# Kernel tuning notes

Measured on AMD Instinct MI355X. Metric: run time of the kernel, lower is better.

The kernel has to match this reference:

```python
import jax, jax.numpy as jnp
import numpy as np

VIN, VOUT, E, H = 32000, 32000, 1024, 1024
TS, TT, B = 50, 48, 64


def _lstm_scan(x, m, Wih, Whh, bih, bhh):
    """Masked (packed-sequence-equivalent) LSTM. x:(T,B,E), m:(T,B) bool valid."""
    Bn, Hn = x.shape[1], Whh.shape[1]

    def step(carry, tm):
        h, c = carry
        xt, mt = tm
        gates = xt @ Wih.T + bih + h @ Whh.T + bhh
        i, f, g, o = jnp.split(gates, 4, axis=-1)  # torch gate order i,f,g,o
        c_new = jax.nn.sigmoid(f) * c + jax.nn.sigmoid(i) * jnp.tanh(g)
        h_new = jax.nn.sigmoid(o) * jnp.tanh(c_new)
        mt_ = mt[:, None]
        return (jnp.where(mt_, h_new, h), jnp.where(mt_, c_new, c)), jnp.where(mt_, h_new, 0.0)

    init = (jnp.zeros((Bn, Hn), x.dtype), jnp.zeros((Bn, Hn), x.dtype))
    (h, c), outs = jax.lax.scan(step, init, (x, m))
    return outs, h, c


def setup_inputs() -> dict:
    key = jax.random.key(0)
    ks = jax.random.split(key, 32)
    s = 0.02
    src = jax.random.randint(ks[0], (TS, B), 0, VIN)
    src_len = jnp.sort(jax.random.randint(ks[1], (B,), TS // 2, TS + 1))[::-1]
    src_len = src_len.at[0].set(TS)  # pad_packed pads to max length in batch
    trg = jax.random.randint(ks[2], (TT, B), 0, VOUT)
    p = lambda k, shp: jax.random.normal(k, shp, jnp.float32) * s
    return {
        "src": src, "src_len": src_len, "trg": trg,
        "enc_emb": p(ks[3], (VIN, E)),
        "Wih_f": p(ks[4], (4 * H, E)), "Whh_f": p(ks[5], (4 * H, H)),
        "bih_f": p(ks[6], (4 * H,)), "bhh_f": p(ks[7], (4 * H,)),
        "Wih_b": p(ks[8], (4 * H, E)), "Whh_b": p(ks[9], (4 * H, H)),
        "bih_b": p(ks[10], (4 * H,)), "bhh_b": p(ks[11], (4 * H,)),
        "Wfch": p(ks[12], (H, 2 * H)), "bfch": p(ks[13], (H,)),
        "Wfcc": p(ks[14], (H, 2 * H)), "bfcc": p(ks[15], (H,)),
        "dec_emb": p(ks[16], (VOUT, H)),
        "Wih_d": p(ks[17], (4 * H, 2 * H)), "Whh_d": p(ks[18], (4 * H, H)),
        "bih_d": p(ks[19], (4 * H,)), "bhh_d": p(ks[20], (4 * H,)),
        "Wattn": p(ks[21], (H, 2 * H)), "battn": p(ks[22], (H,)),
        "Wcomb": p(ks[23], (H, 3 * H)), "bcomb": p(ks[24], (H,)),
        "Wout": p(ks[25], (VOUT, H)), "bout": p(ks[26], (VOUT,)),
    }


def reference(src, src_len, trg, enc_emb, Wih_f, Whh_f, bih_f, bhh_f,
              Wih_b, Whh_b, bih_b, bhh_b, Wfch, bfch, Wfcc, bfcc, dec_emb,
              Wih_d, Whh_d, bih_d, bhh_d, Wattn, battn, Wcomb, bcomb, Wout, bout):
    T, Bn = src.shape
    emb = enc_emb[src]                                      # (T,B,E)
    m = jnp.arange(T)[:, None] < src_len[None, :]           # (T,B) valid
    outs_f, hf, cf = _lstm_scan(emb, m, Wih_f, Whh_f, bih_f, bhh_f)
    outs_b, hb, cb = _lstm_scan(emb[::-1], m[::-1], Wih_b, Whh_b, bih_b, bhh_b)
    outs_b = outs_b[::-1]
    enc_outputs = jnp.concatenate([outs_f, outs_b], -1).transpose(1, 0, 2)  # (B,T,2H)
    hidden = jnp.concatenate([hf, hb], -1) @ Wfch.T + bfch  # (B,H)
    cell = jnp.concatenate([cf, cb], -1) @ Wfcc.T + bfcc
    mask_pad = ~m.T                                          # (B,T) True at pads

    attn_proj = jnp.einsum('btd,hd->bth', enc_outputs, Wattn) + battn  # (B,T,H)
    dec_emb_seq = dec_emb[trg]                               # (TT,B,H), dropout=eval

    def dstep(carry, emb_t):
        h, c, dout = carry
        x = jnp.concatenate([emb_t, dout], -1)               # (B, H+H)
        gates = x @ Wih_d.T + bih_d + h @ Whh_d.T + bhh_d
        i, f, g, o = jnp.split(gates, 4, axis=-1)
        c_new = jax.nn.sigmoid(f) * c + jax.nn.sigmoid(i) * jnp.tanh(g)
        h_new = jax.nn.sigmoid(o) * jnp.tanh(c_new)
        scores = jnp.einsum('bth,bh->bt', attn_proj, h_new)
        scores = jnp.where(mask_pad, -jnp.inf, scores)
        w = jax.nn.softmax(scores, -1)
        ctx = jnp.einsum('bt,btd->bd', w, enc_outputs)       # (B,2H)
        dout_new = jnp.concatenate([ctx, h_new], -1) @ Wcomb.T + bcomb
        logits = jax.nn.relu(dout_new) @ Wout.T + bout       # (B,VOUT)
        return (h_new, c_new, dout_new), logits

    init = (hidden, cell, jnp.zeros_like(hidden))
    _, logits = jax.lax.scan(dstep, init, dec_emb_seq[:-1])  # (TT-1,B,V)
    return logits.transpose(1, 2, 0)                         # (B,V,TT-1)
```

## Files before the change

kernel.cpp:

```cpp
#include <hip/hip_runtime.h>
#include <hip/hip_bf16.h>
#include <math.h>


typedef __attribute__((ext_vector_type(8))) short short8;
typedef __attribute__((ext_vector_type(4))) float floatx4;
typedef unsigned short u16;

#define DEV static __device__ __forceinline__

DEV float bf2f(u16 u){ union{unsigned int i; float f;} v; v.i = ((unsigned int)u)<<16; return v.f; }
DEV u16 f2bf(float f){
  union{float f; unsigned int i;} v; v.f = f;
  unsigned int i = v.i;
  return (u16)((i + 0x7fffu + ((i>>16)&1u)) >> 16);
}
DEV float sigm(float x){ return 1.f/(1.f+expf(-x)); }

__global__ __launch_bounds__(256) void cvt2d(const float* __restrict__ src, long sld,
                                             u16* __restrict__ dst, long dld, long cols)
{
  long r = blockIdx.x;
  long c = ((long)blockIdx.y*256 + threadIdx.x)*4;
  if (c >= cols) return;
  const float4 v = *(const float4*)(src + r*sld + c);
  u16* d = dst + r*dld + c;
  d[0]=f2bf(v.x); d[1]=f2bf(v.y); d[2]=f2bf(v.z); d[3]=f2bf(v.w);
}

DEV void split_store(const float4 v, u16* d, u16* e){
  u16 h0=f2bf(v.x), h1=f2bf(v.y), h2=f2bf(v.z), h3=f2bf(v.w);
  d[0]=h0; d[1]=h1; d[2]=h2; d[3]=h3;
  e[0]=f2bf(v.x-bf2f(h0)); e[1]=f2bf(v.y-bf2f(h1));
  e[2]=f2bf(v.z-bf2f(h2)); e[3]=f2bf(v.w-bf2f(h3));
}

__global__ __launch_bounds__(256) void cvtA(
    const float* s0, const float* s1, const float* s2, const float* s3,
    u16* h0, u16* h1, u16* h2, u16* h3,
    u16* l0, u16* l1, u16* l2, u16* l3)
{
  const float* s; u16* h; u16* l;
  switch (blockIdx.z){
    case 0: s=s0; h=h0; l=l0; break;
    case 1: s=s1; h=h1; l=l1; break;
    case 2: s=s2; h=h2; l=l2; break;
    default: s=s3; h=h3; l=l3; break;
  }
  long r = blockIdx.x; long c = (long)threadIdx.x*4;
  split_store(*(const float4*)(s + r*1024 + c), h + r*1024 + c, l + r*1024 + c);
}

__global__ __launch_bounds__(256) void cvtB(
    const float* s0, long sld0, const float* s1, long sld1,
    const float* s2, long sld2, const float* s3, long sld3,
    u16* h0, u16* h1, u16* h2, u16* h3,
    u16* l0, u16* l1, u16* l2, u16* l3)
{
  const float* s; u16* h; u16* l; long sld;
  switch (blockIdx.z){
    case 0: s=s0; h=h0; l=l0; sld=sld0; break;
    case 1: s=s1; h=h1; l=l1; sld=sld1; break;
    case 2: s=s2; h=h2; l=l2; sld=sld2; break;
    default: s=s3; h=h3; l=l3; sld=sld3; break;
  }
  long r = blockIdx.x;
  long c = ((long)blockIdx.y*256 + threadIdx.x)*4;
  split_store(*(const float4*)(s + r*sld + c), h + r*2048 + c, l + r*2048 + c);
}

__global__ __launch_bounds__(256) void cvtC(
    const float* s0, long sld0, u16* h0, u16* l0, long dld0,
    const float* s1, long sld1, u16* h1, u16* l1, long dld1,
    const float* s2, long sld2, u16* h2, u16* l2, long dld2)
{
  const float* s; u16* h; u16* l; long sld, dld;
  switch (blockIdx.z){
    case 0: s=s0; h=h0; l=l0; sld=sld0; dld=dld0; break;
    case 1: s=s1; h=h1; l=l1; sld=sld1; dld=dld1; break;
    default: s=s2; h=h2; l=l2; sld=sld2; dld=dld2; break;
  }
  long r = blockIdx.x; long c = (long)threadIdx.x*4;
  split_store(*(const float4*)(s + r*sld + c), h + r*dld + c, l + r*dld + c);
}

__global__ __launch_bounds__(256) void cvt_cell_split(const float* __restrict__ c_all,
                                                      u16* __restrict__ hi, u16* __restrict__ lo)
{
  int b = blockIdx.x, tid = threadIdx.x;
  for (int k = 0; k < 8; k++){
    int u = tid + k*256;
    int dir = u >> 10, uu = u & 1023;
    float v = c_all[dir*65536 + b*1024 + uu];
    u16 h = f2bf(v);
    hi[b*2048 + u] = h;
    lo[b*2048 + u] = f2bf(v - bf2f(h));
  }
}

__global__ __launch_bounds__(256) void bias_combine(
    const float* a1,const float* a2,float* o1,
    const float* b1,const float* b2,float* o2,
    const float* c1,const float* c2,float* o3,
    const float* battn, float* o4)
{
  int i = blockIdx.x*256 + threadIdx.x;
  if (i < 4096){ o1[i]=a1[i]+a2[i]; o2[i]=b1[i]+b2[i]; o3[i]=c1[i]+c2[i]; }
  if (i < 2048) o4[i] = (i < 1024) ? battn[i] : 0.f;
}

__global__ __launch_bounds__(256) void zero_u32(unsigned int* p, int n){
  int i = blockIdx.x*256 + threadIdx.x;
  if (i < n) p[i] = 0;
}

__global__ __launch_bounds__(256) void gather_embed_split(const int* __restrict__ idx,
                                                          const float* __restrict__ tab,
                                                          u16* __restrict__ hi, u16* __restrict__ lo)
{
  int r = blockIdx.x, tid = threadIdx.x;
  int tok = idx[r];
  float4 v = ((const float4*)(tab + (long)tok*1024))[tid];
  split_store(v, hi + (long)r*1024 + tid*4, lo + (long)r*1024 + tid*4);
}

template<int AS, int BS>
__global__ __launch_bounds__(256) void gemm128(
    const u16* __restrict__ Ahi, const u16* __restrict__ Alo, int lda,
    const u16* __restrict__ Bhi, const u16* __restrict__ Blo, int ldb,
    int M, int N, int K,
    const float* __restrict__ bias,
    float* __restrict__ Cf, int ldc)
{
  __shared__ u16 Ash[128][36];
  __shared__ u16 Bsh[128][36];
  __shared__ u16 Asl[AS?128:1][36];
  __shared__ u16 Bsl[BS?128:1][36];
  const int tid = threadIdx.x;
  const int lane = tid & 63;
  const int w = tid >> 6, wm = w >> 1, wn = w & 1;
  const int m0 = blockIdx.x * 128;
  const int n0 = blockIdx.y * 128;

  floatx4 acc[4][4];
  #pragma unroll
  for (int i=0;i<4;i++)
    #pragma unroll
    for (int j=0;j<4;j++) acc[i][j] = (floatx4)0.f;

  const int seg = tid & 3;
  const int rowh = tid >> 2;
  const int nk = K >> 5;
  for (int kk = 0; kk < nk; kk++) {
    int kbase = kk*32 + seg*8;
    #pragma unroll
    for (int p=0;p<2;p++){
      int r = rowh + p*64;
      bool okA = (m0 + r < M);
      int4 va = okA ? *(const int4*)(Ahi + (long)(m0+r)*lda + kbase) : make_int4(0,0,0,0);
      *(int4*)&Ash[r][seg*8] = va;
      if (AS){
        int4 vl = okA ? *(const int4*)(Alo + (long)(m0+r)*lda + kbase) : make_int4(0,0,0,0);
        *(int4*)&Asl[r][seg*8] = vl;
      }
      *(int4*)&Bsh[r][seg*8] = *(const int4*)(Bhi + (long)(n0+r)*ldb + kbase);
      if (BS)
        *(int4*)&Bsl[r][seg*8] = *(const int4*)(Blo + (long)(n0+r)*ldb + kbase);
    }
    __syncthreads();
    short8 ah[4], bh[4], al[4], bl[4];
    #pragma unroll
    for (int i=0;i<4;i++){
      ah[i] = *(const short8*)&Ash[wm*64 + i*16 + (lane&15)][(lane>>4)*8];
      if (AS) al[i] = *(const short8*)&Asl[wm*64 + i*16 + (lane&15)][(lane>>4)*8];
    }
    #pragma unroll
    for (int j=0;j<4;j++){
      bh[j] = *(const short8*)&Bsh[wn*64 + j*16 + (lane&15)][(lane>>4)*8];
      if (BS) bl[j] = *(const short8*)&Bsl[wn*64 + j*16 + (lane&15)][(lane>>4)*8];
    }
    #pragma unroll
    for (int i=0;i<4;i++)
      #pragma unroll
      for (int j=0;j<4;j++){
        acc[i][j] = __builtin_amdgcn_mfma_f32_16x16x32_bf16(ah[i], bh[j], acc[i][j], 0,0,0);
        if (AS) acc[i][j] = __builtin_amdgcn_mfma_f32_16x16x32_bf16(al[i], bh[j], acc[i][j], 0,0,0);
        if (BS) acc[i][j] = __builtin_amdgcn_mfma_f32_16x16x32_bf16(ah[i], bl[j], acc[i][j], 0,0,0);
      }
    __syncthreads();
  }
  const int rb0 = (lane>>4)*4, cf = lane & 15;
  #pragma unroll
  for (int i=0;i<4;i++){
    #pragma unroll
    for (int j=0;j<4;j++){
      int n = n0 + wn*64 + j*16 + cf;
      #pragma unroll
      for (int r=0;r<4;r++){
        int m = m0 + wm*64 + i*16 + rb0 + r;
        if (m >= M) continue;
        Cf[(long)m*ldc + n] = acc[i][j][r] + (bias ? bias[n] : 0.f);
      }
    }
  }
}

template<int MODE>
__global__ __launch_bounds__(256) void gemm64(
    const u16* __restrict__ Ahi, const u16* __restrict__ Alo, int lda,
    const u16* __restrict__ Bhi, const u16* __restrict__ Blo, int ldb,
    int K, const float* __restrict__ bias,
    float* __restrict__ outF,
    u16* __restrict__ o1hi, u16* __restrict__ o1lo)
{
  __shared__ u16 Ash[64][36], Asl[64][36];
  __shared__ u16 Bsh[64][36], Bsl[64][36];
  const int tid = threadIdx.x, lane = tid&63, w = tid>>6;
  const int n0 = blockIdx.x * 64;
  floatx4 acc[4];
  #pragma unroll
  for (int i=0;i<4;i++) acc[i]=(floatx4)0.f;
  const int seg = tid&3, row = tid>>2;
  const int nk = K>>5;
  for (int kk=0; kk<nk; kk++){
    int kbase = kk*32 + seg*8;
    *(int4*)&Ash[row][seg*8] = *(const int4*)(Ahi + (long)row*lda + kbase);
    *(int4*)&Asl[row][seg*8] = *(const int4*)(Alo + (long)row*lda + kbase);
    *(int4*)&Bsh[row][seg*8] = *(const int4*)(Bhi + (long)(n0+row)*ldb + kbase);
    *(int4*)&Bsl[row][seg*8] = *(const int4*)(Blo + (long)(n0+row)*ldb + kbase);
    __syncthreads();
    short8 bh = *(const short8*)&Bsh[w*16 + (lane&15)][(lane>>4)*8];
    short8 bl = *(const short8*)&Bsl[w*16 + (lane&15)][(lane>>4)*8];
    #pragma unroll
    for (int i=0;i<4;i++){
      short8 ah = *(const short8*)&Ash[i*16 + (lane&15)][(lane>>4)*8];
      short8 al = *(const short8*)&Asl[i*16 + (lane&15)][(lane>>4)*8];
      acc[i] = __builtin_amdgcn_mfma_f32_16x16x32_bf16(ah, bh, acc[i], 0,0,0);
      acc[i] = __builtin_amdgcn_mfma_f32_16x16x32_bf16(al, bh, acc[i], 0,0,0);
      acc[i] = __builtin_amdgcn_mfma_f32_16x16x32_bf16(ah, bl, acc[i], 0,0,0);
    }
    __syncthreads();
  }
  const int rb0 = (lane>>4)*4, cf = lane&15;
  int n = n0 + w*16 + cf;
  #pragma unroll
  for (int i=0;i<4;i++){
    #pragma unroll
    for (int r=0;r<4;r++){
      int m = i*16 + rb0 + r;
      float v = acc[i][r] + bias[n];
      if (MODE == 0){
        u16 h = f2bf(v), l = f2bf(v - bf2f(h));
        o1hi[m*2048 + n] = h; o1lo[m*2048 + n] = l;
      } else {
        outF[m*1024 + n] = v;
      }
    }
  }
}

__global__ __launch_bounds__(512) void enc_step(
    int s,
    const u16* __restrict__ hin_hi, const u16* __restrict__ hin_lo,
    u16* __restrict__ hout_hi, u16* __restrict__ hout_lo,
    float* __restrict__ c_all,
    const u16* __restrict__ Whhf_hi, const u16* __restrict__ Whhf_lo,
    const u16* __restrict__ Whhb_hi, const u16* __restrict__ Whhb_lo,
    const float* __restrict__ Gfb,
    const float* __restrict__ bias_f, const float* __restrict__ bias_b,
    const int* __restrict__ src_len,
    u16* __restrict__ eo_hi, u16* __restrict__ eo_lo)
{
  __shared__ u16 Ah[32][1032], Al[32][1032];
  __shared__ float gl[4][32][17];
  const int tid = threadIdx.x, lane = tid&63, w = tid>>6;
  const int b0  = (blockIdx.x >> 7) * 32;
  const int dir = (blockIdx.x >> 6) & 1;
  const int u0  = (blockIdx.x & 63) * 16;
  const u16* Whh_hi = dir ? Whhb_hi : Whhf_hi;
  const u16* Whh_lo = dir ? Whhb_lo : Whhf_lo;
  const float* bias = dir ? bias_b : bias_f;
  const int trow = dir ? (49 - s) : s;

  {
    int row = tid>>4, c0 = (tid&15)*8;
    const u16* sh = hin_hi + dir*1024 + (long)(b0+row)*2048;
    const u16* sl = hin_lo + dir*1024 + (long)(b0+row)*2048;
    #pragma unroll
    for (int j=0;j<8;j++){
      int c = c0 + j*128;
      *(int4*)&Ah[row][c] = *(const int4*)(sh + c);
      *(int4*)&Al[row][c] = *(const int4*)(sl + c);
    }
  }
  __syncthreads();

  const int g = w & 3;
  const int rh = (w >> 2) * 16;
  const int lane15 = lane & 15;
  const int cseg = (lane>>4)*8;
  const int rowb = g*1024 + u0 + lane15;
  const u16* bhp = Whh_hi + (long)rowb*1024 + cseg;
  const u16* blp = Whh_lo + (long)rowb*1024 + cseg;

  floatx4 accA = (floatx4)0.f, accB = (floatx4)0.f;
  #pragma unroll 4
  for (int kk=0; kk<32; kk+=2){
    int k0 = kk*32, k1 = k0 + 32;
    short8 bh0 = *(const short8*)(bhp + k0);
    short8 bl0 = *(const short8*)(blp + k0);
    short8 ah0 = *(const short8*)&Ah[rh + lane15][k0 + cseg];
    short8 al0 = *(const short8*)&Al[rh + lane15][k0 + cseg];
    accA = __builtin_amdgcn_mfma_f32_16x16x32_bf16(ah0, bh0, accA, 0,0,0);
    accA = __builtin_amdgcn_mfma_f32_16x16x32_bf16(al0, bh0, accA, 0,0,0);
    accA = __builtin_amdgcn_mfma_f32_16x16x32_bf16(ah0, bl0, accA, 0,0,0);
    short8 bh1 = *(const short8*)(bhp + k1);
    short8 bl1 = *(const short8*)(blp + k1);
    short8 ah1 = *(const short8*)&Ah[rh + lane15][k1 + cseg];
    short8 al1 = *(const short8*)&Al[rh + lane15][k1 + cseg];
    accB = __builtin_amdgcn_mfma_f32_16x16x32_bf16(ah1, bh1, accB, 0,0,0);
    accB = __builtin_amdgcn_mfma_f32_16x16x32_bf16(al1, bh1, accB, 0,0,0);
    accB = __builtin_amdgcn_mfma_f32_16x16x32_bf16(ah1, bl1, accB, 0,0,0);
  }
  floatx4 acc = accA + accB;
  const int rb0 = (lane>>4)*4;
  #pragma unroll
  for (int r=0;r<4;r++)
    gl[g][rh + rb0 + r][lane15] = acc[r];
  __syncthreads();
  {
    int bl_ = tid >> 4, u = tid & 15;
    int b = b0 + bl_, uu = u0 + u;
    long grow = (long)(trow*64 + b)*8192 + dir*4096;
    float gi = gl[0][bl_][u] + Gfb[grow +        uu] + bias[uu];
    float gf = gl[1][bl_][u] + Gfb[grow + 1024 + uu] + bias[1024+uu];
    float gg2 = gl[2][bl_][u] + Gfb[grow + 2048 + uu] + bias[2048+uu];
    float go = gl[3][bl_][u] + Gfb[grow + 3072 + uu] + bias[3072+uu];
    float c_old = c_all[dir*65536 + b*1024 + uu];
    float c_new = sigm(gf)*c_old + sigm(gi)*tanhf(gg2);
    float h_new = sigm(go)*tanhf(c_new);
    bool valid = trow < src_len[b];
    if (valid) c_all[dir*65536 + b*1024 + uu] = c_new;
    u16 hh = f2bf(h_new);
    u16 hl = f2bf(h_new - bf2f(hh));
    int hidx = b*2048 + dir*1024 + uu;
    hout_hi[hidx] = valid ? hh : hin_hi[hidx];
    hout_lo[hidx] = valid ? hl : hin_lo[hidx];
    long eidx = (long)(b*50 + trow)*2048 + dir*1024 + uu;
    eo_hi[eidx] = valid ? hh : (u16)0;
    eo_lo[eidx] = valid ? hl : (u16)0;
  }
}

__global__ __launch_bounds__(512) void dec_gates(
    int t,
    const u16* __restrict__ ain_hi, const u16* __restrict__ ain_lo,
    u16* __restrict__ aout_hi, u16* __restrict__ aout_lo,
    float* __restrict__ c_dec,
    const u16* __restrict__ Wcat_hi, const u16* __restrict__ Wcat_lo,
    const float* __restrict__ Gd,
    const float* __restrict__ bias_d,
    float* __restrict__ hf32)
{
  __shared__ u16 Ah[16][2056], Al[16][2056];
  __shared__ float gl[8][16][17];
  const int tid=threadIdx.x, lane=tid&63, w=tid>>6;
  const int b0 = (blockIdx.x >> 6) * 16;
  const int u0 = (blockIdx.x & 63) * 16;

  {
    int row = tid>>5, c0 = (tid&31)*8;
    const u16* sh = ain_hi + (long)(b0+row)*2048;
    const u16* sl = ain_lo + (long)(b0+row)*2048;
    #pragma unroll
    for (int j=0;j<8;j++){
      int c = c0 + j*256;
      *(int4*)&Ah[row][c] = *(const int4*)(sh + c);
      *(int4*)&Al[row][c] = *(const int4*)(sl + c);
    }
  }
  __syncthreads();

  const int g = w & 3;
  const int kh = (w >> 2) * 1024;
  const int lane15 = lane & 15;
  const int cseg = (lane>>4)*8;
  const int rowb = g*1024 + u0 + lane15;
  const u16* bhp = Wcat_hi + (long)rowb*2048 + kh + cseg;
  const u16* blp = Wcat_lo + (long)rowb*2048 + kh + cseg;

  floatx4 accA = (floatx4)0.f, accB = (floatx4)0.f;
  #pragma unroll 4
  for (int kk=0; kk<32; kk+=2){
    int k0 = kk*32, k1 = k0 + 32;
    short8 bh0 = *(const short8*)(bhp + k0);
    short8 bl0 = *(const short8*)(blp + k0);
    short8 ah0 = *(const short8*)&Ah[lane15][kh + k0 + cseg];
    short8 al0 = *(const short8*)&Al[lane15][kh + k0 + cseg];
    accA = __builtin_amdgcn_mfma_f32_16x16x32_bf16(ah0,bh0,accA,0,0,0);
    accA = __builtin_amdgcn_mfma_f32_16x16x32_bf16(al0,bh0,accA,0,0,0);
    accA = __builtin_amdgcn_mfma_f32_16x16x32_bf16(ah0,bl0,accA,0,0,0);
    short8 bh1 = *(const short8*)(bhp + k1);
    short8 bl1 = *(const short8*)(blp + k1);
    short8 ah1 = *(const short8*)&Ah[lane15][kh + k1 + cseg];
    short8 al1 = *(const short8*)&Al[lane15][kh + k1 + cseg];
    accB = __builtin_amdgcn_mfma_f32_16x16x32_bf16(ah1,bh1,accB,0,0,0);
    accB = __builtin_amdgcn_mfma_f32_16x16x32_bf16(al1,bh1,accB,0,0,0);
    accB = __builtin_amdgcn_mfma_f32_16x16x32_bf16(ah1,bl1,accB,0,0,0);
  }
  floatx4 acc = accA + accB;
  const int rb0=(lane>>4)*4;
  #pragma unroll
  for(int r=0;r<4;r++) gl[w][rb0+r][lane15] = acc[r];
  __syncthreads();
  if (tid < 256){
    int bl_ = tid>>4, u = tid&15;
    int b = b0 + bl_, uu = u0 + u;
    long grow = (long)(t*64 + b)*4096;
    float gi = gl[0][bl_][u] + gl[4][bl_][u] + Gd[grow +        uu] + bias_d[uu];
    float gf = gl[1][bl_][u] + gl[5][bl_][u] + Gd[grow + 1024 + uu] + bias_d[1024+uu];
    float gg2 = gl[2][bl_][u] + gl[6][bl_][u] + Gd[grow + 2048 + uu] + bias_d[2048+uu];
    float go = gl[3][bl_][u] + gl[7][bl_][u] + Gd[grow + 3072 + uu] + bias_d[3072+uu];
    float c_old = c_dec[b*1024+uu];
    float c_new = sigm(gf)*c_old + sigm(gi)*tanhf(gg2);
    float h_new = sigm(go)*tanhf(c_new);
    c_dec[b*1024+uu] = c_new;
    u16 hh = f2bf(h_new);
    u16 hl = f2bf(h_new - bf2f(hh));
    aout_hi[b*2048 + uu] = hh;  aout_lo[b*2048 + uu] = hl;
    hf32[b*1024 + uu] = h_new;
  }
}

__global__ __launch_bounds__(256) void attn_w(
    const float* __restrict__ APf,
    const float* __restrict__ hf32,
    const int* __restrict__ src_len,
    float* __restrict__ wout)
{
  __shared__ float h_sh[1024];
  __shared__ float sc_sh[50];
  const int tid = threadIdx.x, lane = tid&63, w = tid>>6;
  const int b = blockIdx.x;
  for (int i = tid; i < 1024; i += 256) h_sh[i] = hf32[b*1024 + i];
  __syncthreads();
  for (int tp = w; tp < 50; tp += 4){
    const float* ap = APf + (long)(b*50+tp)*2048;
    float p = 0.f;
    #pragma unroll
    for (int i=0;i<16;i++){ int d = lane + i*64; p += ap[d]*h_sh[d]; }
    #pragma unroll
    for (int off=32; off>0; off>>=1) p += __shfl_down(p, off);
    if (lane==0) sc_sh[tp] = p;
  }
  __syncthreads();
  if (w == 0){
    int len = src_len[b];
    float s = (lane < 50 && lane < len) ? sc_sh[lane] : -3.4e38f;
    float mx = s;
    #pragma unroll
    for (int off=32; off>0; off>>=1) mx = fmaxf(mx, __shfl_xor(mx, off));
    float p = (lane < 50 && lane < len) ? expf(s - mx) : 0.f;
    float sum = p;
    #pragma unroll
    for (int off=32; off>0; off>>=1) sum += __shfl_xor(sum, off);
    if (lane < 50) wout[b*50 + lane] = p / sum;
  }
}

__global__ __launch_bounds__(256) void dout_step(
    int t,
    const u16* __restrict__ h_hi, const u16* __restrict__ h_lo,
    const u16* __restrict__ Wch_h, const u16* __restrict__ Wch_l,
    const float* __restrict__ APf,
    const float* __restrict__ wout,
    const float* __restrict__ bcomb,
    u16* __restrict__ ac_hi, u16* __restrict__ ac_lo,
    u16* __restrict__ dall_h)
{
  __shared__ u16 Ash[4][16][36], Asl[4][16][36];
  __shared__ u16 Bsh[4][16][36], Bsl[4][16][36];
  __shared__ float gl[4][16][17];
  const int tid=threadIdx.x, lane=tid&63, w=tid>>6;
  const int b0 = ((blockIdx.x >> 6) & 3) * 16;
  const int n0 = (blockIdx.x & 63) * 16;
  floatx4 acc = (floatx4)0.f;
  const int r = lane&15, sg = lane>>4;
  for (int kk=0; kk<8; kk++){
    int kb = w*256 + kk*32 + sg*8;
    *(int4*)&Ash[w][r][sg*8] = *(const int4*)(h_hi + (b0+r)*2048 + kb);
    *(int4*)&Asl[w][r][sg*8] = *(const int4*)(h_lo + (b0+r)*2048 + kb);
    *(int4*)&Bsh[w][r][sg*8] = *(const int4*)(Wch_h + (long)(n0+r)*1024 + kb);
    *(int4*)&Bsl[w][r][sg*8] = *(const int4*)(Wch_l + (long)(n0+r)*1024 + kb);
    __syncthreads();
    short8 ah = *(const short8*)&Ash[w][lane&15][(lane>>4)*8];
    short8 al = *(const short8*)&Asl[w][lane&15][(lane>>4)*8];
    short8 bh = *(const short8*)&Bsh[w][lane&15][(lane>>4)*8];
    short8 bl = *(const short8*)&Bsl[w][lane&15][(lane>>4)*8];
    acc = __builtin_amdgcn_mfma_f32_16x16x32_bf16(ah,bh,acc,0,0,0);
    acc = __builtin_amdgcn_mfma_f32_16x16x32_bf16(al,bh,acc,0,0,0);
    acc = __builtin_amdgcn_mfma_f32_16x16x32_bf16(ah,bl,acc,0,0,0);
    __syncthreads();
  }
  const int rb0=(lane>>4)*4, cf=lane&15;
  #pragma unroll
  for(int rr=0;rr<4;rr++) gl[w][rb0+rr][cf] = acc[rr];
  __syncthreads();
  {
    int bl_ = tid>>4, nl = tid&15;
    int b = b0 + bl_, nn = n0 + nl;
    float v = gl[0][bl_][nl]+gl[1][bl_][nl]+gl[2][bl_][nl]+gl[3][bl_][nl] + bcomb[nn];
    const float* wp = wout + b*50;
    const float* Pp = APf + (long)(b*50)*2048 + 1024 + nn;
    for (int tp=0; tp<50; tp++) v += wp[tp] * Pp[(long)tp*2048];
    u16 h = f2bf(v), l = f2bf(v - bf2f(h));
    ac_hi[b*2048 + 1024 + nn] = h;  ac_lo[b*2048 + 1024 + nn] = l;
    float rv = v > 0.f ? v : 0.f;
    dall_h[(long)(b*47 + t)*1024 + nn] = f2bf(rv);
  }
}

__global__ __launch_bounds__(256) void logits_gemm(
    const u16* __restrict__ Wout_bf,
    const u16* __restrict__ dall_h,
    const float* __restrict__ bout,
    float* __restrict__ out)
{
  const int x = blockIdx.x;
  const int y = blockIdx.y;
  const int cnt = (x < 5) ? 16 : 15;
  if (y >= cnt*32) return;
  const int vt = ((x < 5) ? x*16 : 80 + (x-5)*15) + (y >> 5);
  const int b0 = (y & 31)*2;
  const int v0 = vt * 256;

  __shared__ u16 Wsh[256][36];
  __shared__ u16 Dh[2][48][36];
  const int tid = threadIdx.x, lane = tid&63, w = tid>>6;
  floatx4 acc[2][4][3];
  #pragma unroll
  for (int bb=0;bb<2;bb++)
    #pragma unroll
    for (int i=0;i<4;i++)
      #pragma unroll
      for (int j=0;j<3;j++) acc[bb][i][j]=(floatx4)0.f;
  const int lrow = tid>>1, lseg = tid&1;
  for (int kk=0; kk<32; kk++){
    int kb = kk*32;
    #pragma unroll
    for (int p=0;p<2;p++){
      int row = lrow + p*128;
      const u16* src = Wout_bf + (long)(v0+row)*1024 + kb + lseg*16;
      *(int4*)&Wsh[row][lseg*16]     = *(const int4*)(src);
      *(int4*)&Wsh[row][lseg*16 + 8] = *(const int4*)(src + 8);
    }
    if (tid < 192){
      int bb = tid/96, t2 = tid - bb*96;
      int row = t2>>1, sg = t2&1;
      long a = (long)((b0+bb)*47+row)*1024 + kb + sg*16;
      *(int4*)&Dh[bb][row][sg*16]     = *(const int4*)(dall_h + a);
      *(int4*)&Dh[bb][row][sg*16 + 8] = *(const int4*)(dall_h + a + 8);
    }
    __syncthreads();
    short8 av[4];
    #pragma unroll
    for (int i=0;i<4;i++)
      av[i] = *(const short8*)&Wsh[w*64 + i*16 + (lane&15)][(lane>>4)*8];
    #pragma unroll
    for (int j=0;j<3;j++){
      #pragma unroll
      for (int bb=0;bb<2;bb++){
        short8 bh = *(const short8*)&Dh[bb][j*16 + (lane&15)][(lane>>4)*8];
        #pragma unroll
        for (int i=0;i<4;i++)
          acc[bb][i][j] = __builtin_amdgcn_mfma_f32_16x16x32_bf16(av[i], bh, acc[bb][i][j], 0,0,0);
      }
    }
    __syncthreads();
  }
  const int rb0=(lane>>4)*4, cf=lane&15;
  #pragma unroll
  for (int bb=0;bb<2;bb++){
    #pragma unroll
    for (int i=0;i<4;i++){
      #pragma unroll
      for (int j=0;j<3;j++){
        int tt = j*16 + cf;
        if (tt >= 47) continue;
        #pragma unroll
        for (int r=0;r<4;r++){
          int v = v0 + w*64 + i*16 + rb0 + r;
          out[(long)(b0+bb)*1504000 + (long)v*47 + tt] = acc[bb][i][j][r] + bout[v];
        }
      }
    }
  }
}

extern "C" void kernel_launch(void* const* d_in, const int* in_sizes, int n_in,
                              void* d_out, int out_size, void* d_ws, size_t ws_size,
                              hipStream_t stream)
{
  (void)in_sizes; (void)n_in; (void)out_size; (void)ws_size;
  const int*   src     = (const int*)d_in[0];
  const int*   src_len = (const int*)d_in[1];
  const int*   trg     = (const int*)d_in[2];
  const float* enc_emb = (const float*)d_in[3];
  const float* Wih_f   = (const float*)d_in[4];
  const float* Whh_f   = (const float*)d_in[5];
  const float* bih_f   = (const float*)d_in[6];
  const float* bhh_f   = (const float*)d_in[7];
  const float* Wih_b   = (const float*)d_in[8];
  const float* Whh_b   = (const float*)d_in[9];
  const float* bih_b   = (const float*)d_in[10];
  const float* bhh_b   = (const float*)d_in[11];
  const float* Wfch    = (const float*)d_in[12];
  const float* bfch    = (const float*)d_in[13];
  const float* Wfcc    = (const float*)d_in[14];
  const float* bfcc    = (const float*)d_in[15];
  const float* dec_emb = (const float*)d_in[16];
  const float* Wih_d   = (const float*)d_in[17];
  const float* Whh_d   = (const float*)d_in[18];
  const float* bih_d   = (const float*)d_in[19];
  const float* bhh_d   = (const float*)d_in[20];
  const float* Wattn   = (const float*)d_in[21];
  const float* battn   = (const float*)d_in[22];
  const float* Wcomb   = (const float*)d_in[23];
  const float* bcomb   = (const float*)d_in[24];
  const float* Wout    = (const float*)d_in[25];
  const float* bout    = (const float*)d_in[26];
  float* out = (float*)d_out;

  size_t off = 0;
  auto alloc = [&](size_t bytes)->void*{
    void* p = (char*)d_ws + off; off += (bytes + 255) & ~(size_t)255; return p; };

  u16* Wenc_h = (u16*)alloc((size_t)8192*1024*2);  u16* Wenc_l = (u16*)alloc((size_t)8192*1024*2);
  u16* Whhf_h = (u16*)alloc((size_t)4096*1024*2);  u16* Whhf_l = (u16*)alloc((size_t)4096*1024*2);
  u16* Whhb_h = (u16*)alloc((size_t)4096*1024*2);  u16* Whhb_l = (u16*)alloc((size_t)4096*1024*2);
  u16* WihdA_h= (u16*)alloc((size_t)4096*1024*2);  u16* WihdA_l= (u16*)alloc((size_t)4096*1024*2);
  u16* Wcat_h = (u16*)alloc((size_t)4096*2048*2);  u16* Wcat_l = (u16*)alloc((size_t)4096*2048*2);
  u16* Wfch_h = (u16*)alloc((size_t)1024*2048*2);  u16* Wfch_l = (u16*)alloc((size_t)1024*2048*2);
  u16* Wfcc_h = (u16*)alloc((size_t)1024*2048*2);  u16* Wfcc_l = (u16*)alloc((size_t)1024*2048*2);
  u16* Wap_h  = (u16*)alloc((size_t)2048*2048*2);  u16* Wap_l  = (u16*)alloc((size_t)2048*2048*2);
  u16* Wch_h  = (u16*)alloc((size_t)1024*1024*2);  u16* Wch_l  = (u16*)alloc((size_t)1024*1024*2);
  u16* Wout_bf =(u16*)alloc((size_t)32000*1024*2);
  u16* embx_h = (u16*)alloc((size_t)3200*1024*2);  u16* embx_l = (u16*)alloc((size_t)3200*1024*2);
  u16* dembx_h= (u16*)alloc((size_t)3008*1024*2);  u16* dembx_l= (u16*)alloc((size_t)3008*1024*2);
  float* Gfb  = (float*)alloc((size_t)3200*8192*4);
  float* Gd   = (float*)alloc((size_t)3008*4096*4);
  u16* eo_h  = (u16*)alloc((size_t)3200*2048*2);
  u16* eo_l  = (u16*)alloc((size_t)3200*2048*2);
  u16* h0_h  = (u16*)alloc((size_t)64*2048*2);  u16* h0_l  = (u16*)alloc((size_t)64*2048*2);
  u16* h1_h  = (u16*)alloc((size_t)64*2048*2);  u16* h1_l  = (u16*)alloc((size_t)64*2048*2);
  u16* cfin_h= (u16*)alloc((size_t)64*2048*2);  u16* cfin_l= (u16*)alloc((size_t)64*2048*2);
  u16* ac0_h = (u16*)alloc((size_t)64*2048*2);  u16* ac0_l = (u16*)alloc((size_t)64*2048*2);
  u16* ac1_h = (u16*)alloc((size_t)64*2048*2);  u16* ac1_l = (u16*)alloc((size_t)64*2048*2);
  u16* dall_h= (u16*)alloc((size_t)3009*1024*2);
  float* APf   = (float*)alloc((size_t)3200*2048*4);
  float* c_enc = (float*)alloc((size_t)2*64*1024*4);
  float* c_dec = (float*)alloc((size_t)64*1024*4);
  float* hf32  = (float*)alloc((size_t)64*1024*4);
  float* wout  = (float*)alloc((size_t)64*50*4);
  float* bias_f = (float*)alloc(4096*4);
  float* bias_b = (float*)alloc(4096*4);
  float* bias_d = (float*)alloc(4096*4);
  float* bias_ap= (float*)alloc(2048*4);

  cvtA<<<dim3(4096,1,4),256,0,stream>>>(Wih_f, Wih_b, Whh_f, Whh_b,
                                        Wenc_h, Wenc_h + (size_t)4096*1024, Whhf_h, Whhb_h,
                                        Wenc_l, Wenc_l + (size_t)4096*1024, Whhf_l, Whhb_l);
  cvtB<<<dim3(1024,2,4),256,0,stream>>>(Wfch, 2048, Wfcc, 2048, Wattn, 2048, Wcomb, 3072,
                                        Wfch_h, Wfcc_h, Wap_h, Wap_h + (size_t)1024*2048,
                                        Wfch_l, Wfcc_l, Wap_l, Wap_l + (size_t)1024*2048);
  cvtC<<<dim3(4096,1,3),256,0,stream>>>(Wih_d, 2048, WihdA_h, WihdA_l, 1024,
                                        Whh_d, 1024, Wcat_h, Wcat_l, 2048,
                                        Wih_d + 1024, 2048, Wcat_h + 1024, Wcat_l + 1024, 2048);
  cvtC<<<dim3(1024,1,1),256,0,stream>>>(Wcomb + 2048, 3072, Wch_h, Wch_l, 1024,
                                        Wcomb + 2048, 3072, Wch_h, Wch_l, 1024,
                                        Wcomb + 2048, 3072, Wch_h, Wch_l, 1024);
  cvt2d<<<dim3(32000,1),256,0,stream>>>(Wout, 1024, Wout_bf, 1024, 1024);
  bias_combine<<<16,256,0,stream>>>(bih_f,bhh_f,bias_f, bih_b,bhh_b,bias_b, bih_d,bhh_d,bias_d, battn,bias_ap);

  gather_embed_split<<<3200,256,0,stream>>>(src, enc_emb, embx_h, embx_l);
  gather_embed_split<<<3008,256,0,stream>>>(trg, dec_emb, dembx_h, dembx_l);

  zero_u32<<<256,256,0,stream>>>((unsigned int*)h0_h, 65536);
  zero_u32<<<256,256,0,stream>>>((unsigned int*)h0_l, 65536);
  zero_u32<<<256,256,0,stream>>>((unsigned int*)ac0_h, 65536);
  zero_u32<<<256,256,0,stream>>>((unsigned int*)ac0_l, 65536);
  zero_u32<<<512,256,0,stream>>>((unsigned int*)c_enc, 131072);

  gemm128<1,1><<<dim3(25,64),256,0,stream>>>(embx_h, embx_l, 1024, Wenc_h, Wenc_l, 1024, 3200, 8192, 1024, nullptr, Gfb, 8192);
  gemm128<1,1><<<dim3(24,32),256,0,stream>>>(dembx_h, dembx_l, 1024, WihdA_h, WihdA_l, 1024, 3008, 4096, 1024, nullptr, Gd, 4096);

  u16* hh_[2] = {h0_h, h1_h};
  u16* hl_[2] = {h0_l, h1_l};
  for (int s=0; s<50; s++)
    enc_step<<<256,512,0,stream>>>(s, hh_[s&1], hl_[s&1], hh_[(s+1)&1], hl_[(s+1)&1], c_enc,
                                   Whhf_h, Whhf_l, Whhb_h, Whhb_l, Gfb, bias_f, bias_b, src_len, eo_h, eo_l);

  cvt_cell_split<<<64,256,0,stream>>>(c_enc, cfin_h, cfin_l);

  gemm128<1,1><<<dim3(25,16),256,0,stream>>>(eo_h, eo_l, 2048, Wap_h, Wap_l, 2048, 3200, 2048, 2048, bias_ap, APf, 2048);

  gemm64<0><<<16,256,0,stream>>>(h0_h, h0_l, 2048, Wfch_h, Wfch_l, 2048, 2048, bfch, nullptr, ac0_h, ac0_l);
  gemm64<1><<<16,256,0,stream>>>(cfin_h, cfin_l, 2048, Wfcc_h, Wfcc_l, 2048, 2048, bfcc, c_dec, nullptr, nullptr);

  u16* ah_[2] = {ac0_h, ac1_h};
  u16* al_[2] = {ac0_l, ac1_l};
  for (int t=0; t<47; t++){
    int cur = t&1, nxt = (t+1)&1;
    dec_gates<<<256,512,0,stream>>>(t, ah_[cur], al_[cur], ah_[nxt], al_[nxt], c_dec,
                                    Wcat_h, Wcat_l, Gd, bias_d, hf32);
    attn_w<<<64,256,0,stream>>>(APf, hf32, src_len, wout);
    dout_step<<<256,256,0,stream>>>(t, ah_[nxt], al_[nxt], Wch_h, Wch_l, APf, wout, bcomb,
                                    ah_[nxt], al_[nxt], dall_h);
  }

  logits_gemm<<<dim3(8,512),256,0,stream>>>(Wout_bf, dall_h, bout, out);
}
```

Measured before the change: 4.261 ms.

## Split recurrent LSTM steps over more blocks and move decoder gate math into attention

```diff
diff --git a/kernel.cpp b/kernel.cpp
--- a/kernel.cpp
+++ b/kernel.cpp
@@ -271,10 +271,10 @@
     const int* __restrict__ src_len,
     u16* __restrict__ eo_hi, u16* __restrict__ eo_lo)
 {
-  __shared__ u16 Ah[32][1032], Al[32][1032];
-  __shared__ float gl[4][32][17];
+  __shared__ u16 Ah[16][1032];
+  __shared__ float gl[8][16][17];
   const int tid = threadIdx.x, lane = tid&63, w = tid>>6;
-  const int b0  = (blockIdx.x >> 7) * 32;
+  const int b0  = (blockIdx.x >> 7) * 16;
   const int dir = (blockIdx.x >> 6) & 1;
   const int u0  = (blockIdx.x & 63) * 16;
   const u16* Whh_hi = dir ? Whhb_hi : Whhf_hi;
@@ -283,41 +283,40 @@
   const int trow = dir ? (49 - s) : s;
 
   {
-    int row = tid>>4, c0 = (tid&15)*8;
+    int row = tid>>5, c0 = (tid&31)*8;
     const u16* sh = hin_hi + dir*1024 + (long)(b0+row)*2048;
-    const u16* sl = hin_lo + dir*1024 + (long)(b0+row)*2048;
-    #pragma unroll
-    for (int j=0;j<8;j++){
-      int c = c0 + j*128;
+    #pragma unroll
+    for (int j=0;j<4;j++){
+      int c = c0 + j*256;
       *(int4*)&Ah[row][c] = *(const int4*)(sh + c);
-      *(int4*)&Al[row][c] = *(const int4*)(sl + c);
     }
   }
   __syncthreads();
 
-  const int g = w & 3;
-  const int rh = (w >> 2) * 16;
+  const int g  = w & 3;
+  const int kh = (w >> 2) * 512;
   const int lane15 = lane & 15;
   const int cseg = (lane>>4)*8;
   const int rowb = g*1024 + u0 + lane15;
-  const u16* bhp = Whh_hi + (long)rowb*1024 + cseg;
-  const u16* blp = Whh_lo + (long)rowb*1024 + cseg;
+  const u16* bhp = Whh_hi + (long)rowb*1024 + kh + cseg;
+  const u16* blp = Whh_lo + (long)rowb*1024 + kh + cseg;
+  const u16* alp = hin_lo + dir*1024 + (long)(b0+lane15)*2048 + kh + cseg;
 
   floatx4 accA = (floatx4)0.f, accB = (floatx4)0.f;
   #pragma unroll 4
-  for (int kk=0; kk<32; kk+=2){
+  for (int kk=0; kk<16; kk+=2){
     int k0 = kk*32, k1 = k0 + 32;
     short8 bh0 = *(const short8*)(bhp + k0);
     short8 bl0 = *(const short8*)(blp + k0);
-    short8 ah0 = *(const short8*)&Ah[rh + lane15][k0 + cseg];
-    short8 al0 = *(const short8*)&Al[rh + lane15][k0 + cseg];
+    short8 ah0 = *(const short8*)&Ah[lane15][kh + k0 + cseg];
+    short8 al0 = *(const short8*)(alp + k0);
     accA = __builtin_amdgcn_mfma_f32_16x16x32_bf16(ah0, bh0, accA, 0,0,0);
     accA = __builtin_amdgcn_mfma_f32_16x16x32_bf16(al0, bh0, accA, 0,0,0);
     accA = __builtin_amdgcn_mfma_f32_16x16x32_bf16(ah0, bl0, accA, 0,0,0);
     short8 bh1 = *(const short8*)(bhp + k1);
     short8 bl1 = *(const short8*)(blp + k1);
-    short8 ah1 = *(const short8*)&Ah[rh + lane15][k1 + cseg];
-    short8 al1 = *(const short8*)&Al[rh + lane15][k1 + cseg];
+    short8 ah1 = *(const short8*)&Ah[lane15][kh + k1 + cseg];
+    short8 al1 = *(const short8*)(alp + k1);
     accB = __builtin_amdgcn_mfma_f32_16x16x32_bf16(ah1, bh1, accB, 0,0,0);
     accB = __builtin_amdgcn_mfma_f32_16x16x32_bf16(al1, bh1, accB, 0,0,0);
     accB = __builtin_amdgcn_mfma_f32_16x16x32_bf16(ah1, bl1, accB, 0,0,0);
@@ -325,17 +324,16 @@
   floatx4 acc = accA + accB;
   const int rb0 = (lane>>4)*4;
   #pragma unroll
-  for (int r=0;r<4;r++)
-    gl[g][rh + rb0 + r][lane15] = acc[r];
+  for (int r=0;r<4;r++) gl[w][rb0+r][lane15] = acc[r];
   __syncthreads();
-  {
+  if (tid < 256){
     int bl_ = tid >> 4, u = tid & 15;
     int b = b0 + bl_, uu = u0 + u;
     long grow = (long)(trow*64 + b)*8192 + dir*4096;
-    float gi = gl[0][bl_][u] + Gfb[grow +        uu] + bias[uu];
-    float gf = gl[1][bl_][u] + Gfb[grow + 1024 + uu] + bias[1024+uu];
-    float gg2 = gl[2][bl_][u] + Gfb[grow + 2048 + uu] + bias[2048+uu];
-    float go = gl[3][bl_][u] + Gfb[grow + 3072 + uu] + bias[3072+uu];
+    float gi = gl[0][bl_][u] + gl[4][bl_][u] + Gfb[grow +        uu] + bias[uu];
+    float gf = gl[1][bl_][u] + gl[5][bl_][u] + Gfb[grow + 1024 + uu] + bias[1024+uu];
+    float gg2 = gl[2][bl_][u] + gl[6][bl_][u] + Gfb[grow + 2048 + uu] + bias[2048+uu];
+    float go = gl[3][bl_][u] + gl[7][bl_][u] + Gfb[grow + 3072 + uu] + bias[3072+uu];
     float c_old = c_all[dir*65536 + b*1024 + uu];
     float c_new = sigm(gf)*c_old + sigm(gi)*tanhf(gg2);
     float h_new = sigm(go)*tanhf(c_new);
@@ -352,58 +350,53 @@
   }
 }
 
-__global__ __launch_bounds__(512) void dec_gates(
-    int t,
+__global__ __launch_bounds__(512) void dec_part(
     const u16* __restrict__ ain_hi, const u16* __restrict__ ain_lo,
-    u16* __restrict__ aout_hi, u16* __restrict__ aout_lo,
-    float* __restrict__ c_dec,
     const u16* __restrict__ Wcat_hi, const u16* __restrict__ Wcat_lo,
-    const float* __restrict__ Gd,
-    const float* __restrict__ bias_d,
-    float* __restrict__ hf32)
-{
-  __shared__ u16 Ah[16][2056], Al[16][2056];
+    float* __restrict__ gpart)
+{
+  __shared__ u16 Ah[16][1032];
   __shared__ float gl[8][16][17];
   const int tid=threadIdx.x, lane=tid&63, w=tid>>6;
-  const int b0 = (blockIdx.x >> 6) * 16;
-  const int u0 = (blockIdx.x & 63) * 16;
+  const int b0  = (blockIdx.x >> 7) * 16;
+  const int khB = ((blockIdx.x >> 6) & 1) * 1024;
+  const int u0  = (blockIdx.x & 63) * 16;
 
   {
     int row = tid>>5, c0 = (tid&31)*8;
-    const u16* sh = ain_hi + (long)(b0+row)*2048;
-    const u16* sl = ain_lo + (long)(b0+row)*2048;
-    #pragma unroll
-    for (int j=0;j<8;j++){
+    const u16* sh = ain_hi + (long)(b0+row)*2048 + khB;
+    #pragma unroll
+    for (int j=0;j<4;j++){
       int c = c0 + j*256;
       *(int4*)&Ah[row][c] = *(const int4*)(sh + c);
-      *(int4*)&Al[row][c] = *(const int4*)(sl + c);
     }
   }
   __syncthreads();
 
-  const int g = w & 3;
-  const int kh = (w >> 2) * 1024;
+  const int g  = w & 3;
+  const int kq = (w >> 2) * 512;
   const int lane15 = lane & 15;
   const int cseg = (lane>>4)*8;
   const int rowb = g*1024 + u0 + lane15;
-  const u16* bhp = Wcat_hi + (long)rowb*2048 + kh + cseg;
-  const u16* blp = Wcat_lo + (long)rowb*2048 + kh + cseg;
+  const u16* bhp = Wcat_hi + (long)rowb*2048 + khB + kq + cseg;
+  const u16* blp = Wcat_lo + (long)rowb*2048 + khB + kq + cseg;
+  const u16* alp = ain_lo + (long)(b0+lane15)*2048 + khB + kq + cseg;
 
   floatx4 accA = (floatx4)0.f, accB = (floatx4)0.f;
   #pragma unroll 4
-  for (int kk=0; kk<32; kk+=2){
+  for (int kk=0; kk<16; kk+=2){
     int k0 = kk*32, k1 = k0 + 32;
     short8 bh0 = *(const short8*)(bhp + k0);
     short8 bl0 = *(const short8*)(blp + k0);
-    short8 ah0 = *(const short8*)&Ah[lane15][kh + k0 + cseg];
-    short8 al0 = *(const short8*)&Al[lane15][kh + k0 + cseg];
+    short8 ah0 = *(const short8*)&Ah[lane15][kq + k0 + cseg];
+    short8 al0 = *(const short8*)(alp + k0);
     accA = __builtin_amdgcn_mfma_f32_16x16x32_bf16(ah0,bh0,accA,0,0,0);
     accA = __builtin_amdgcn_mfma_f32_16x16x32_bf16(al0,bh0,accA,0,0,0);
     accA = __builtin_amdgcn_mfma_f32_16x16x32_bf16(ah0,bl0,accA,0,0,0);
     short8 bh1 = *(const short8*)(bhp + k1);
     short8 bl1 = *(const short8*)(blp + k1);
-    short8 ah1 = *(const short8*)&Ah[lane15][kh + k1 + cseg];
-    short8 al1 = *(const short8*)&Al[lane15][kh + k1 + cseg];
+    short8 ah1 = *(const short8*)&Ah[lane15][kq + k1 + cseg];
+    short8 al1 = *(const short8*)(alp + k1);
     accB = __builtin_amdgcn_mfma_f32_16x16x32_bf16(ah1,bh1,accB,0,0,0);
     accB = __builtin_amdgcn_mfma_f32_16x16x32_bf16(al1,bh1,accB,0,0,0);
     accB = __builtin_amdgcn_mfma_f32_16x16x32_bf16(ah1,bl1,accB,0,0,0);
@@ -416,25 +409,22 @@
   if (tid < 256){
     int bl_ = tid>>4, u = tid&15;
     int b = b0 + bl_, uu = u0 + u;
-    long grow = (long)(t*64 + b)*4096;
-    float gi = gl[0][bl_][u] + gl[4][bl_][u] + Gd[grow +        uu] + bias_d[uu];
-    float gf = gl[1][bl_][u] + gl[5][bl_][u] + Gd[grow + 1024 + uu] + bias_d[1024+uu];
-    float gg2 = gl[2][bl_][u] + gl[6][bl_][u] + Gd[grow + 2048 + uu] + bias_d[2048+uu];
-    float go = gl[3][bl_][u] + gl[7][bl_][u] + Gd[grow + 3072 + uu] + bias_d[3072+uu];
-    float c_old = c_dec[b*1024+uu];
-    float c_new = sigm(gf)*c_old + sigm(gi)*tanhf(gg2);
-    float h_new = sigm(go)*tanhf(c_new);
-    c_dec[b*1024+uu] = c_new;
-    u16 hh = f2bf(h_new);
-    u16 hl = f2bf(h_new - bf2f(hh));
-    aout_hi[b*2048 + uu] = hh;  aout_lo[b*2048 + uu] = hl;
-    hf32[b*1024 + uu] = h_new;
-  }
-}
-
-__global__ __launch_bounds__(256) void attn_w(
+    float* gp = gpart + (khB>>10)*262144 + b*4096;
+    gp[       uu] = gl[0][bl_][u] + gl[4][bl_][u];
+    gp[1024 + uu] = gl[1][bl_][u] + gl[5][bl_][u];
+    gp[2048 + uu] = gl[2][bl_][u] + gl[6][bl_][u];
+    gp[3072 + uu] = gl[3][bl_][u] + gl[7][bl_][u];
+  }
+}
+
+__global__ __launch_bounds__(256) void attn_gates(
+    int t,
+    const float* __restrict__ gpart,
+    const float* __restrict__ Gd,
+    const float* __restrict__ bias_d,
+    float* __restrict__ c_dec,
+    u16* __restrict__ ac_hi, u16* __restrict__ ac_lo,
     const float* __restrict__ APf,
-    const float* __restrict__ hf32,
     const int* __restrict__ src_len,
     float* __restrict__ wout)
 {
@@ -442,8 +432,28 @@
   __shared__ float sc_sh[50];
   const int tid = threadIdx.x, lane = tid&63, w = tid>>6;
   const int b = blockIdx.x;
-  for (int i = tid; i < 1024; i += 256) h_sh[i] = hf32[b*1024 + i];
+
+  {
+    const float* gp0 = gpart + b*4096;
+    const float* gp1 = gpart + 262144 + b*4096;
+    long grow = (long)(t*64 + b)*4096;
+    for (int u = tid; u < 1024; u += 256){
+      float gi = gp0[       u] + gp1[       u] + Gd[grow +        u] + bias_d[u];
+      float gf = gp0[1024 + u] + gp1[1024 + u] + Gd[grow + 1024 + u] + bias_d[1024+u];
+      float gg2= gp0[2048 + u] + gp1[2048 + u] + Gd[grow + 2048 + u] + bias_d[2048+u];
+      float go = gp0[3072 + u] + gp1[3072 + u] + Gd[grow + 3072 + u] + bias_d[3072+u];
+      float c_old = c_dec[b*1024 + u];
+      float c_new = sigm(gf)*c_old + sigm(gi)*tanhf(gg2);
+      float h_new = sigm(go)*tanhf(c_new);
+      c_dec[b*1024 + u] = c_new;
+      u16 hh = f2bf(h_new);
+      ac_hi[b*2048 + u] = hh;
+      ac_lo[b*2048 + u] = f2bf(h_new - bf2f(hh));
+      h_sh[u] = h_new;
+    }
+  }
   __syncthreads();
+
   for (int tp = w; tp < 50; tp += 4){
     const float* ap = APf + (long)(b*50+tp)*2048;
     float p = 0.f;
@@ -535,8 +545,9 @@
   const int v0 = vt * 256;
 
   __shared__ u16 Wsh[256][36];
-  __shared__ u16 Dh[2][48][36];
   const int tid = threadIdx.x, lane = tid&63, w = tid>>6;
+  const int lane15 = lane & 15;
+  const int cseg = (lane>>4)*8;
   floatx4 acc[2][4][3];
   #pragma unroll
   for (int bb=0;bb<2;bb++)
@@ -545,6 +556,8 @@
       #pragma unroll
       for (int j=0;j<3;j++) acc[bb][i][j]=(floatx4)0.f;
   const int lrow = tid>>1, lseg = tid&1;
+  const u16* dp0 = dall_h + (long)(b0*47 + lane15)*1024 + cseg;
+  const u16* dp1 = dall_h + (long)((b0+1)*47 + lane15)*1024 + cseg;
   for (int kk=0; kk<32; kk++){
     int kb = kk*32;
     #pragma unroll
@@ -554,26 +567,19 @@
       *(int4*)&Wsh[row][lseg*16]     = *(const int4*)(src);
       *(int4*)&Wsh[row][lseg*16 + 8] = *(const int4*)(src + 8);
     }
-    if (tid < 192){
-      int bb = tid/96, t2 = tid - bb*96;
-      int row = t2>>1, sg = t2&1;
-      long a = (long)((b0+bb)*47+row)*1024 + kb + sg*16;
-      *(int4*)&Dh[bb][row][sg*16]     = *(const int4*)(dall_h + a);
-      *(int4*)&Dh[bb][row][sg*16 + 8] = *(const int4*)(dall_h + a + 8);
-    }
     __syncthreads();
     short8 av[4];
     #pragma unroll
     for (int i=0;i<4;i++)
-      av[i] = *(const short8*)&Wsh[w*64 + i*16 + (lane&15)][(lane>>4)*8];
+      av[i] = *(const short8*)&Wsh[w*64 + i*16 + lane15][cseg];
     #pragma unroll
     for (int j=0;j<3;j++){
+      short8 bh0 = *(const short8*)(dp0 + (long)j*16*1024 + kb);
+      short8 bh1 = *(const short8*)(dp1 + (long)j*16*1024 + kb);
       #pragma unroll
-      for (int bb=0;bb<2;bb++){
-        short8 bh = *(const short8*)&Dh[bb][j*16 + (lane&15)][(lane>>4)*8];
-        #pragma unroll
-        for (int i=0;i<4;i++)
-          acc[bb][i][j] = __builtin_amdgcn_mfma_f32_16x16x32_bf16(av[i], bh, acc[bb][i][j], 0,0,0);
+      for (int i=0;i<4;i++){
+        acc[0][i][j] = __builtin_amdgcn_mfma_f32_16x16x32_bf16(av[i], bh0, acc[0][i][j], 0,0,0);
+        acc[1][i][j] = __builtin_amdgcn_mfma_f32_16x16x32_bf16(av[i], bh1, acc[1][i][j], 0,0,0);
       }
     }
     __syncthreads();
@@ -658,9 +664,9 @@
   u16* ac1_h = (u16*)alloc((size_t)64*2048*2);  u16* ac1_l = (u16*)alloc((size_t)64*2048*2);
   u16* dall_h= (u16*)alloc((size_t)3009*1024*2);
   float* APf   = (float*)alloc((size_t)3200*2048*4);
+  float* gpart = (float*)alloc((size_t)2*64*4096*4);
   float* c_enc = (float*)alloc((size_t)2*64*1024*4);
   float* c_dec = (float*)alloc((size_t)64*1024*4);
-  float* hf32  = (float*)alloc((size_t)64*1024*4);
   float* wout  = (float*)alloc((size_t)64*50*4);
   float* bias_f = (float*)alloc(4096*4);
   float* bias_b = (float*)alloc(4096*4);
@@ -697,7 +703,7 @@
   u16* hh_[2] = {h0_h, h1_h};
   u16* hl_[2] = {h0_l, h1_l};
   for (int s=0; s<50; s++)
-    enc_step<<<256,512,0,stream>>>(s, hh_[s&1], hl_[s&1], hh_[(s+1)&1], hl_[(s+1)&1], c_enc,
+    enc_step<<<512,512,0,stream>>>(s, hh_[s&1], hl_[s&1], hh_[(s+1)&1], hl_[(s+1)&1], c_enc,
                                    Whhf_h, Whhf_l, Whhb_h, Whhb_l, Gfb, bias_f, bias_b, src_len, eo_h, eo_l);
 
   cvt_cell_split<<<64,256,0,stream>>>(c_enc, cfin_h, cfin_l);
@@ -711,9 +717,9 @@
   u16* al_[2] = {ac0_l, ac1_l};
   for (int t=0; t<47; t++){
     int cur = t&1, nxt = (t+1)&1;
-    dec_gates<<<256,512,0,stream>>>(t, ah_[cur], al_[cur], ah_[nxt], al_[nxt], c_dec,
-                                    Wcat_h, Wcat_l, Gd, bias_d, hf32);
-    attn_w<<<64,256,0,stream>>>(APf, hf32, src_len, wout);
+    dec_part<<<512,512,0,stream>>>(ah_[cur], al_[cur], Wcat_h, Wcat_l, gpart);
+    attn_gates<<<64,256,0,stream>>>(t, gpart, Gd, bias_d, c_dec,
+                                    ah_[nxt], al_[nxt], APf, src_len, wout);
     dout_step<<<256,256,0,stream>>>(t, ah_[nxt], al_[nxt], Wch_h, Wch_l, APf, wout, bcomb,
                                     ah_[nxt], al_[nxt], dall_h);
   }
```

After: 5.184 ms. 1.22x slower.
